# Optimization experiments

Measured on AMD Instinct MI355X. Metric: run time of the kernel, lower is better.

Reference implementation:

```python
import jax, jax.numpy as jnp
import numpy as np

N_NODES = 50000
N_EDGES = 800000
F_IN, F_HID, F_OUT = 128, 64, 32


def setup_inputs() -> dict:
    key = jax.random.key(0)
    k1, k2, k3, k4, k5, k6 = jax.random.split(key, 6)
    x = jax.random.normal(k1, (N_NODES, F_IN), dtype=jnp.float32)
    edge_index = jax.random.randint(k2, (2, N_EDGES), 0, N_NODES, dtype=jnp.int64)
    # Glorot-ish init for the two GCNConv linear layers
    W1 = jax.random.normal(k3, (F_IN, F_HID), dtype=jnp.float32) / np.sqrt(F_IN)
    b1 = jnp.zeros((F_HID,), dtype=jnp.float32)
    W2 = jax.random.normal(k4, (F_HID, F_OUT), dtype=jnp.float32) / np.sqrt(F_HID)
    b2 = jnp.zeros((F_OUT,), dtype=jnp.float32)
    return {"x": x, "edge_index": edge_index, "W1": W1, "b1": b1, "W2": W2, "b2": b2}


def _gcn_conv(x, src, dst, norm, W, b):
    # GCNConv: linear transform, then D^{-1/2}(A+I)D^{-1/2} aggregation
    xw = x @ W                                # [N, F_out]
    msg = xw[src] * norm[:, None]             # [E+N, F_out] gather + scale
    out = jax.ops.segment_sum(msg, dst, num_segments=x.shape[0])
    return out + b


def reference(x, edge_index, W1, b1, W2, b2):
    n = x.shape[0]
    self_loops = jnp.arange(n, dtype=edge_index.dtype)
    src = jnp.concatenate([edge_index[0], self_loops])  # [E+N]
    dst = jnp.concatenate([edge_index[1], self_loops])
    # symmetric degree normalization (self-loops guarantee deg >= 1)
    deg = jax.ops.segment_sum(jnp.ones_like(dst, dtype=x.dtype), dst, num_segments=n)
    dinv = jax.lax.rsqrt(deg)
    norm = dinv[src] * dinv[dst]              # [E+N]

    h = _gcn_conv(x, src, dst, norm, W1, b1)
    h = jax.nn.relu(h)
    # dropout p=0.5 is identity in eval mode (training=False)
    out = _gcn_conv(h, src, dst, norm, W2, b2)
    return out
```

## Files before the change

kernel.cpp:

```cpp
#include <hip/hip_runtime.h>
#include <hip/hip_fp16.h>

#define NN 50000
#define NE 800000
#define F_IN 128
#define F_HID 64
#define F_OUT 32
#define CAP 48
#define NBUCK 196
#define EPB 4096
#define CELL 64
#define NXW1 782

typedef _Float16 f16x8 __attribute__((ext_vector_type(8)));
typedef float f32x4 __attribute__((ext_vector_type(4)));
#define XS_STR 136


__global__ __launch_bounds__(256) void fused_xw1_partition_kernel(
        const float* __restrict__ x, const float* __restrict__ W,
        const int* __restrict__ src, const int* __restrict__ dst,
        int* __restrict__ cnt2t, unsigned int* __restrict__ bstore2,
        __half* __restrict__ outh) {
    __shared__ _Float16 xs[64 * XS_STR];
    __shared__ _Float16 wt[64 * XS_STR];
    __shared__ int hist[4][NBUCK];
    __shared__ int cur[NBUCK];
    int t = threadIdx.x;

    if (blockIdx.x < NBUCK) {
        int blk = blockIdx.x;
        for (int i = t; i < 4 * NBUCK; i += 256) ((int*)hist)[i] = 0;
        __syncthreads();
        int wv = t >> 6;
        int base = blk * EPB;
        unsigned int pk[16];
#pragma unroll
        for (int i = 0; i < 16; ++i) {
            int e = base + i * 256 + t;
            if (e < NE) {
                unsigned int d = (unsigned int)dst[e];
                unsigned int s = (unsigned int)src[e];
                pk[i] = (d << 16) | s;
                atomicAdd(&hist[wv][d >> 8], 1);
            } else {
                pk[i] = 0xFFFFFFFFu;
            }
        }
        __syncthreads();
        for (int b = t; b < NBUCK; b += 256) {
            int h = hist[0][b] + hist[1][b] + hist[2][b] + hist[3][b];
            cur[b] = 0;
            cnt2t[b * NBUCK + blk] = h;
        }
        __syncthreads();
#pragma unroll
        for (int i = 0; i < 16; ++i) {
            unsigned int p = pk[i];
            if (p != 0xFFFFFFFFu) {
                int b = p >> 24;
                int pos = atomicAdd(&cur[b], 1);
                if (pos < CELL) bstore2[((size_t)blk * NBUCK + b) * CELL + pos] = p;
            }
        }
        return;
    }

    int node0 = (blockIdx.x - NBUCK) * 64;

    {
        int r = t >> 2;
        int c0 = (t & 3) * 32;
        int gn = node0 + r;
        if (gn > NN - 1) gn = NN - 1;
        const float4* xrow = (const float4*)(x + (size_t)gn * F_IN);
#pragma unroll
        for (int i = 0; i < 8; ++i) {
            float4 v = xrow[(c0 >> 2) + i];
            _Float16* p = &xs[r * XS_STR + c0 + i * 4];
            p[0] = (_Float16)v.x; p[1] = (_Float16)v.y;
            p[2] = (_Float16)v.z; p[3] = (_Float16)v.w;
        }
    }
#pragma unroll
    for (int i = 0; i < 8; ++i) {
        int idx4 = t + i * 256;
        int k = idx4 >> 4;
        int n0 = (idx4 & 15) << 2;
        float4 v = ((const float4*)W)[idx4];
        wt[(n0 + 0) * XS_STR + k] = (_Float16)v.x;
        wt[(n0 + 1) * XS_STR + k] = (_Float16)v.y;
        wt[(n0 + 2) * XS_STR + k] = (_Float16)v.z;
        wt[(n0 + 3) * XS_STR + k] = (_Float16)v.w;
    }
    __syncthreads();

    int wave = t >> 6;
    int l = t & 63;
    int quad = l >> 4;
    int lm = l & 15;

    f32x4 acc[4] = {{0,0,0,0},{0,0,0,0},{0,0,0,0},{0,0,0,0}};
    const _Float16* abase = &xs[(wave * 16 + lm) * XS_STR + quad * 8];
#pragma unroll
    for (int kk4 = 0; kk4 < 4; ++kk4) {
        int kk = kk4 * 32;
        f16x8 a = *(const f16x8*)(abase + kk);
#pragma unroll
        for (int ft = 0; ft < 4; ++ft) {
            f16x8 b = *(const f16x8*)&wt[(ft * 16 + lm) * XS_STR + kk + quad * 8];
            acc[ft] = __builtin_amdgcn_mfma_f32_16x16x32_f16(a, b, acc[ft], 0, 0, 0);
        }
    }

    __syncthreads();
    _Float16* ot = xs;
#pragma unroll
    for (int ft = 0; ft < 4; ++ft) {
#pragma unroll
        for (int r = 0; r < 4; ++r) {
            int row_l = wave * 16 + quad * 4 + r;
            ot[row_l * 64 + ft * 16 + lm] = (_Float16)acc[ft][r];
        }
    }
    __syncthreads();
#pragma unroll
    for (int i = 0; i < 2; ++i) {
        int idx = t + i * 256;
        int row = idx >> 3;
        int c8 = (idx & 7) * 8;
        int gn = node0 + row;
        if (gn < NN)
            *(uint4*)(outh + (size_t)gn * 64 + c8) = *(const uint4*)&ot[row * 64 + c8];
    }
}


__device__ __forceinline__ void slot_insert(unsigned int p, int* cnt_l,
                                            unsigned short* slot_l) {
    int dl = (p >> 16) & 255;
    int pos = atomicAdd(&cnt_l[dl], 1);
    if (pos < CAP) slot_l[dl * CAP + pos] = (unsigned short)(p & 0xFFFFu);
}

__global__ __launch_bounds__(256) void build_slots_kernel(
        const int* __restrict__ cnt2t, const unsigned int* __restrict__ bstore2,
        unsigned short* __restrict__ slot, int* __restrict__ cnt_g, float* __restrict__ dinv) {
    __shared__ unsigned short slot_l[256 * CAP];
    __shared__ int cnt_l[256];
    int t = threadIdx.x;
    int b = blockIdx.x;
    cnt_l[t] = 0;
    __syncthreads();

    for (int blk = t; blk < NBUCK; blk += 256) {
        int c = cnt2t[b * NBUCK + blk];
        if (c > CELL) c = CELL;
        const unsigned int* seg = bstore2 + ((size_t)blk * NBUCK + b) * CELL;
        int j = 0;
        for (; j + 4 <= c; j += 4) {
            unsigned int p0 = seg[j + 0];
            unsigned int p1 = seg[j + 1];
            unsigned int p2 = seg[j + 2];
            unsigned int p3 = seg[j + 3];
            slot_insert(p0, cnt_l, slot_l);
            slot_insert(p1, cnt_l, slot_l);
            slot_insert(p2, cnt_l, slot_l);
            slot_insert(p3, cnt_l, slot_l);
        }
        for (; j < c; ++j) slot_insert(seg[j], cnt_l, slot_l);
    }
    __syncthreads();

    unsigned int* sg = (unsigned int*)(slot + (size_t)b * 256 * CAP);
    const unsigned int* sl = (const unsigned int*)slot_l;
    for (int j = t; j < 256 * CAP / 2; j += 256) sg[j] = sl[j];

    int n = b * 256 + t;
    if (n < NN) {
        int c = cnt_l[t];
        cnt_g[n] = c;
        dinv[n] = rsqrtf(1.0f + (float)c);
    }
}


__global__ __launch_bounds__(256, 6) void gather64_w2_kernel(
        const __half* __restrict__ xw, const int* __restrict__ cnt,
        const unsigned short* __restrict__ slot, const float* __restrict__ dinv,
        const float* __restrict__ b1, const float* __restrict__ W2,
        __half* __restrict__ hw2h) {
    __shared__ float w2s[F_HID * F_OUT];
    __shared__ float hl[4][F_HID];
    int t = threadIdx.x;
    for (int i = t; i < F_HID * F_OUT / 4; i += 256)
        ((float4*)w2s)[i] = ((const float4*)W2)[i];
    __syncthreads();

    int lane = t & 63;
    int wv = t >> 6;
    int n = blockIdx.x * 4 + wv;
    int st = lane >> 4;
    int fl4 = lane & 15;
    const uint2* base = (const uint2*)xw;
    int deg = cnt[n];
    if (deg > CAP) deg = CAP;
    float din = dinv[n];
    const unsigned short* srow = slot + (size_t)n * CAP;
    uint2 u_self = base[(size_t)n * 16 + fl4];
    float4 bb = ((const float4*)b1)[fl4];
    float a0 = 0, a1 = 0, a2 = 0, a3 = 0;
    int e = st;
    for (; e + 12 < deg; e += 16) {
        int s0 = srow[e];
        int s1 = srow[e + 4];
        int s2 = srow[e + 8];
        int s3 = srow[e + 12];
        float dv0 = dinv[s0], dv1 = dinv[s1], dv2 = dinv[s2], dv3 = dinv[s3];
        uint2 u0 = base[(size_t)s0 * 16 + fl4];
        uint2 u1 = base[(size_t)s1 * 16 + fl4];
        uint2 u2 = base[(size_t)s2 * 16 + fl4];
        uint2 u3 = base[(size_t)s3 * 16 + fl4];
        float2 p0 = __half22float2(*(__half2*)&u0.x), p1 = __half22float2(*(__half2*)&u0.y);
        float2 q0 = __half22float2(*(__half2*)&u1.x), q1 = __half22float2(*(__half2*)&u1.y);
        float2 r0 = __half22float2(*(__half2*)&u2.x), r1 = __half22float2(*(__half2*)&u2.y);
        float2 t0 = __half22float2(*(__half2*)&u3.x), t1 = __half22float2(*(__half2*)&u3.y);
        a0 += dv0 * p0.x + dv1 * q0.x + dv2 * r0.x + dv3 * t0.x;
        a1 += dv0 * p0.y + dv1 * q0.y + dv2 * r0.y + dv3 * t0.y;
        a2 += dv0 * p1.x + dv1 * q1.x + dv2 * r1.x + dv3 * t1.x;
        a3 += dv0 * p1.y + dv1 * q1.y + dv2 * r1.y + dv3 * t1.y;
    }
    for (; e < deg; e += 4) {
        int s = srow[e];
        float dv = dinv[s];
        uint2 u = base[(size_t)s * 16 + fl4];
        float2 p0 = __half22float2(*(__half2*)&u.x);
        float2 p1 = __half22float2(*(__half2*)&u.y);
        a0 += dv * p0.x; a1 += dv * p0.y; a2 += dv * p1.x; a3 += dv * p1.y;
    }
    a0 += __shfl_xor(a0, 16, 64); a1 += __shfl_xor(a1, 16, 64);
    a2 += __shfl_xor(a2, 16, 64); a3 += __shfl_xor(a3, 16, 64);
    a0 += __shfl_xor(a0, 32, 64); a1 += __shfl_xor(a1, 32, 64);
    a2 += __shfl_xor(a2, 32, 64); a3 += __shfl_xor(a3, 32, 64);
    if (st == 0) {
        float2 s0 = __half22float2(*(__half2*)&u_self.x);
        float2 s1 = __half22float2(*(__half2*)&u_self.y);
        float v0 = din * (a0 + din * s0.x) + bb.x;
        float v1 = din * (a1 + din * s0.y) + bb.y;
        float v2 = din * (a2 + din * s1.x) + bb.z;
        float v3 = din * (a3 + din * s1.y) + bb.w;
        float* hr = &hl[wv][fl4 * 4];
        hr[0] = v0 > 0.f ? v0 : 0.f;
        hr[1] = v1 > 0.f ? v1 : 0.f;
        hr[2] = v2 > 0.f ? v2 : 0.f;
        hr[3] = v3 > 0.f ? v3 : 0.f;
    }
    asm volatile("s_waitcnt lgkmcnt(0)" ::: "memory");
    {
        int f = lane & 31;
        int kh = lane >> 5;
        const float* hr = &hl[wv][kh * 32];
        float acc = 0.0f;
#pragma unroll
        for (int k = 0; k < 32; ++k) acc += hr[k] * w2s[(kh * 32 + k) * F_OUT + f];
        acc += __shfl_xor(acc, 32, 64);
        if (kh == 0) hw2h[(size_t)n * F_OUT + f] = __float2half(acc * din);
    }
}


__global__ __launch_bounds__(256, 8) void gather32_kernel(
        const __half* __restrict__ scaled, const int* __restrict__ cnt,
        const unsigned short* __restrict__ slot, const float* __restrict__ dinv,
        const float* __restrict__ bias, float* __restrict__ out) {
    int lane = threadIdx.x & 63;
    int n = blockIdx.x * 4 + (threadIdx.x >> 6);
    if (n >= NN) return;
    int st = lane >> 3;
    int fl4 = lane & 7;
    const uint2* base = (const uint2*)scaled;
    int deg = cnt[n];
    if (deg > CAP) deg = CAP;
    const unsigned short* srow = slot + (size_t)n * CAP;
    uint2 u_self = base[(size_t)n * 8 + fl4];
    float4 b4 = ((const float4*)bias)[fl4];
    float a0 = 0, a1 = 0, a2 = 0, a3 = 0;
    int e = st;
    for (; e + 8 < deg; e += 16) {
        int s0 = srow[e];
        int s1 = srow[e + 8];
        uint2 u0 = base[(size_t)s0 * 8 + fl4];
        uint2 u1 = base[(size_t)s1 * 8 + fl4];
        float2 p0 = __half22float2(*(__half2*)&u0.x);
        float2 p1 = __half22float2(*(__half2*)&u0.y);
        float2 q0 = __half22float2(*(__half2*)&u1.x);
        float2 q1 = __half22float2(*(__half2*)&u1.y);
        a0 += p0.x + q0.x; a1 += p0.y + q0.y;
        a2 += p1.x + q1.x; a3 += p1.y + q1.y;
    }
    for (; e < deg; e += 8) {
        int s = srow[e];
        uint2 u = base[(size_t)s * 8 + fl4];
        float2 p0 = __half22float2(*(__half2*)&u.x);
        float2 p1 = __half22float2(*(__half2*)&u.y);
        a0 += p0.x; a1 += p0.y; a2 += p1.x; a3 += p1.y;
    }
    a0 += __shfl_xor(a0, 8, 64);  a1 += __shfl_xor(a1, 8, 64);
    a2 += __shfl_xor(a2, 8, 64);  a3 += __shfl_xor(a3, 8, 64);
    a0 += __shfl_xor(a0, 16, 64); a1 += __shfl_xor(a1, 16, 64);
    a2 += __shfl_xor(a2, 16, 64); a3 += __shfl_xor(a3, 16, 64);
    a0 += __shfl_xor(a0, 32, 64); a1 += __shfl_xor(a1, 32, 64);
    a2 += __shfl_xor(a2, 32, 64); a3 += __shfl_xor(a3, 32, 64);
    if (st == 0) {
        float2 s0 = __half22float2(*(__half2*)&u_self.x);
        float2 s1 = __half22float2(*(__half2*)&u_self.y);
        float di = dinv[n];
        float4 r;
        r.x = di * (a0 + s0.x) + b4.x;
        r.y = di * (a1 + s0.y) + b4.y;
        r.z = di * (a2 + s1.x) + b4.z;
        r.w = di * (a3 + s1.y) + b4.w;
        ((float4*)out)[(size_t)n * 8 + fl4] = r;
    }
}


extern "C" void kernel_launch(void* const* d_in, const int* in_sizes, int n_in,
                              void* d_out, int out_size, void* d_ws, size_t ws_size,
                              hipStream_t stream) {
    const float* x  = (const float*)d_in[0];
    const int*   ei = (const int*)d_in[1];
    const float* W1 = (const float*)d_in[2];
    const float* b1 = (const float*)d_in[3];
    const float* W2 = (const float*)d_in[4];
    const float* b2 = (const float*)d_in[5];
    const int* src = ei;
    const int* dst = ei + NE;

    float*          ws      = (float*)d_ws;
    float*          dinv    = ws;
    int*            cnt     = (int*)(ws + 50048);
    int*            cnt2t   = (int*)(ws + 100096);
    unsigned int*   bstore2 = (unsigned int*)(ws + 138624);
    unsigned short* slot    = (unsigned short*)(ws + 2597248);
    __half*         xw1h    = (__half*)(ws + 3801472);
    __half*         hw2h    = (__half*)(ws + 5401472);
    float*          out     = (float*)d_out;

    fused_xw1_partition_kernel<<<NBUCK + NXW1, 256, 0, stream>>>(
        x, W1, src, dst, cnt2t, bstore2, xw1h);
    build_slots_kernel<<<NBUCK, 256, 0, stream>>>(cnt2t, bstore2, slot, cnt, dinv);
    gather64_w2_kernel<<<NN / 4, 256, 0, stream>>>(xw1h, cnt, slot, dinv, b1, W2, hw2h);
    gather32_kernel<<<NN / 4, 256, 0, stream>>>(hw2h, cnt, slot, dinv, b2, out);
}
```

Baseline: 149.0 us.

## Prescale xw1 by dinv in build_slots and widen gather loads to 16 bytes

The build_slots kernel now multiplies each row of the fp16 xw1 by its node's dinv after computing degrees. This removes the per-edge dinv[src] lookup and multiply in the first gather. Both gather kernels switch from 8-byte to 16-byte loads per lane with eight accumulators, so more edges are in flight per wave but an extra shuffle-reduction step is needed. gather64's occupancy hint goes from 6 to 8. The prescale adds a read-modify-write pass over xw1 inside the serial build_slots kernel and rounds the scaled values to fp16.

```diff
diff --git a/kernel.cpp b/kernel.cpp
--- a/kernel.cpp
+++ b/kernel.cpp
@@ -145,9 +145,11 @@
 
 __global__ __launch_bounds__(256) void build_slots_kernel(
         const int* __restrict__ cnt2t, const unsigned int* __restrict__ bstore2,
-        unsigned short* __restrict__ slot, int* __restrict__ cnt_g, float* __restrict__ dinv) {
+        unsigned short* __restrict__ slot, int* __restrict__ cnt_g,
+        float* __restrict__ dinv, __half* __restrict__ xw) {
     __shared__ unsigned short slot_l[256 * CAP];
     __shared__ int cnt_l[256];
+    __shared__ float dinv_l[256];
     int t = threadIdx.x;
     int b = blockIdx.x;
     cnt_l[t] = 0;
@@ -177,15 +179,38 @@
     for (int j = t; j < 256 * CAP / 2; j += 256) sg[j] = sl[j];
 
     int n = b * 256 + t;
+    float dv = 0.0f;
     if (n < NN) {
         int c = cnt_l[t];
         cnt_g[n] = c;
-        dinv[n] = rsqrtf(1.0f + (float)c);
-    }
-}
-
-
-__global__ __launch_bounds__(256, 6) void gather64_w2_kernel(
+        dv = rsqrtf(1.0f + (float)c);
+        dinv[n] = dv;
+    }
+    dinv_l[t] = dv;
+    __syncthreads();
+
+    {
+        uint4* xb = (uint4*)(xw + (size_t)b * 256 * 64);
+        int rowlim = NN - b * 256;
+        for (int i = t; i < 2048; i += 256) {
+            int row = i >> 3;
+            if (row < rowlim) {
+                uint4 u = xb[i];
+                float s = dinv_l[row];
+                __half2* h2 = (__half2*)&u;
+#pragma unroll
+                for (int j = 0; j < 4; ++j) {
+                    float2 f = __half22float2(h2[j]);
+                    h2[j] = __float22half2_rn(make_float2(f.x * s, f.y * s));
+                }
+                xb[i] = u;
+            }
+        }
+    }
+}
+
+
+__global__ __launch_bounds__(256, 8) void gather64_w2_kernel(
         const __half* __restrict__ xw, const int* __restrict__ cnt,
         const unsigned short* __restrict__ slot, const float* __restrict__ dinv,
         const float* __restrict__ b1, const float* __restrict__ W2,
@@ -200,60 +225,65 @@
     int lane = t & 63;
     int wv = t >> 6;
     int n = blockIdx.x * 4 + wv;
-    int st = lane >> 4;
-    int fl4 = lane & 15;
-    const uint2* base = (const uint2*)xw;
+    int st = lane >> 3;
+    int fl = lane & 7;
+    const uint4* base = (const uint4*)xw;
     int deg = cnt[n];
     if (deg > CAP) deg = CAP;
     float din = dinv[n];
     const unsigned short* srow = slot + (size_t)n * CAP;
-    uint2 u_self = base[(size_t)n * 16 + fl4];
-    float4 bb = ((const float4*)b1)[fl4];
-    float a0 = 0, a1 = 0, a2 = 0, a3 = 0;
+    uint4 u_self = base[(size_t)n * 8 + fl];
+    float a0 = 0, a1 = 0, a2 = 0, a3 = 0, a4 = 0, a5 = 0, a6 = 0, a7 = 0;
     int e = st;
-    for (; e + 12 < deg; e += 16) {
+    for (; e + 8 < deg; e += 16) {
         int s0 = srow[e];
-        int s1 = srow[e + 4];
-        int s2 = srow[e + 8];
-        int s3 = srow[e + 12];
-        float dv0 = dinv[s0], dv1 = dinv[s1], dv2 = dinv[s2], dv3 = dinv[s3];
-        uint2 u0 = base[(size_t)s0 * 16 + fl4];
-        uint2 u1 = base[(size_t)s1 * 16 + fl4];
-        uint2 u2 = base[(size_t)s2 * 16 + fl4];
-        uint2 u3 = base[(size_t)s3 * 16 + fl4];
-        float2 p0 = __half22float2(*(__half2*)&u0.x), p1 = __half22float2(*(__half2*)&u0.y);
-        float2 q0 = __half22float2(*(__half2*)&u1.x), q1 = __half22float2(*(__half2*)&u1.y);
-        float2 r0 = __half22float2(*(__half2*)&u2.x), r1 = __half22float2(*(__half2*)&u2.y);
-        float2 t0 = __half22float2(*(__half2*)&u3.x), t1 = __half22float2(*(__half2*)&u3.y);
-        a0 += dv0 * p0.x + dv1 * q0.x + dv2 * r0.x + dv3 * t0.x;
-        a1 += dv0 * p0.y + dv1 * q0.y + dv2 * r0.y + dv3 * t0.y;
-        a2 += dv0 * p1.x + dv1 * q1.x + dv2 * r1.x + dv3 * t1.x;
-        a3 += dv0 * p1.y + dv1 * q1.y + dv2 * r1.y + dv3 * t1.y;
-    }
-    for (; e < deg; e += 4) {
+        int s1 = srow[e + 8];
+        uint4 u0 = base[(size_t)s0 * 8 + fl];
+        uint4 u1 = base[(size_t)s1 * 8 + fl];
+        float2 p;
+        p = __half22float2(*(__half2*)&u0.x); a0 += p.x; a1 += p.y;
+        p = __half22float2(*(__half2*)&u0.y); a2 += p.x; a3 += p.y;
+        p = __half22float2(*(__half2*)&u0.z); a4 += p.x; a5 += p.y;
+        p = __half22float2(*(__half2*)&u0.w); a6 += p.x; a7 += p.y;
+        p = __half22float2(*(__half2*)&u1.x); a0 += p.x; a1 += p.y;
+        p = __half22float2(*(__half2*)&u1.y); a2 += p.x; a3 += p.y;
+        p = __half22float2(*(__half2*)&u1.z); a4 += p.x; a5 += p.y;
+        p = __half22float2(*(__half2*)&u1.w); a6 += p.x; a7 += p.y;
+    }
+    for (; e < deg; e += 8) {
         int s = srow[e];
-        float dv = dinv[s];
-        uint2 u = base[(size_t)s * 16 + fl4];
-        float2 p0 = __half22float2(*(__half2*)&u.x);
-        float2 p1 = __half22float2(*(__half2*)&u.y);
-        a0 += dv * p0.x; a1 += dv * p0.y; a2 += dv * p1.x; a3 += dv * p1.y;
-    }
-    a0 += __shfl_xor(a0, 16, 64); a1 += __shfl_xor(a1, 16, 64);
-    a2 += __shfl_xor(a2, 16, 64); a3 += __shfl_xor(a3, 16, 64);
-    a0 += __shfl_xor(a0, 32, 64); a1 += __shfl_xor(a1, 32, 64);
-    a2 += __shfl_xor(a2, 32, 64); a3 += __shfl_xor(a3, 32, 64);
+        uint4 u = base[(size_t)s * 8 + fl];
+        float2 p;
+        p = __half22float2(*(__half2*)&u.x); a0 += p.x; a1 += p.y;
+        p = __half22float2(*(__half2*)&u.y); a2 += p.x; a3 += p.y;
+        p = __half22float2(*(__half2*)&u.z); a4 += p.x; a5 += p.y;
+        p = __half22float2(*(__half2*)&u.w); a6 += p.x; a7 += p.y;
+    }
+#define RED64(S) \
+    a0 += __shfl_xor(a0, S, 64); a1 += __shfl_xor(a1, S, 64); \
+    a2 += __shfl_xor(a2, S, 64); a3 += __shfl_xor(a3, S, 64); \
+    a4 += __shfl_xor(a4, S, 64); a5 += __shfl_xor(a5, S, 64); \
+    a6 += __shfl_xor(a6, S, 64); a7 += __shfl_xor(a7, S, 64);
+    RED64(8) RED64(16) RED64(32)
+#undef RED64
     if (st == 0) {
-        float2 s0 = __half22float2(*(__half2*)&u_self.x);
-        float2 s1 = __half22float2(*(__half2*)&u_self.y);
-        float v0 = din * (a0 + din * s0.x) + bb.x;
-        float v1 = din * (a1 + din * s0.y) + bb.y;
-        float v2 = din * (a2 + din * s1.x) + bb.z;
-        float v3 = din * (a3 + din * s1.y) + bb.w;
-        float* hr = &hl[wv][fl4 * 4];
-        hr[0] = v0 > 0.f ? v0 : 0.f;
-        hr[1] = v1 > 0.f ? v1 : 0.f;
-        hr[2] = v2 > 0.f ? v2 : 0.f;
-        hr[3] = v3 > 0.f ? v3 : 0.f;
+        float2 p;
+        p = __half22float2(*(__half2*)&u_self.x); a0 += p.x; a1 += p.y;
+        p = __half22float2(*(__half2*)&u_self.y); a2 += p.x; a3 += p.y;
+        p = __half22float2(*(__half2*)&u_self.z); a4 += p.x; a5 += p.y;
+        p = __half22float2(*(__half2*)&u_self.w); a6 += p.x; a7 += p.y;
+        float4 bb0 = ((const float4*)b1)[fl * 2];
+        float4 bb1 = ((const float4*)b1)[fl * 2 + 1];
+        float* hr = &hl[wv][fl * 8];
+        float v;
+        v = din * a0 + bb0.x; hr[0] = v > 0.f ? v : 0.f;
+        v = din * a1 + bb0.y; hr[1] = v > 0.f ? v : 0.f;
+        v = din * a2 + bb0.z; hr[2] = v > 0.f ? v : 0.f;
+        v = din * a3 + bb0.w; hr[3] = v > 0.f ? v : 0.f;
+        v = din * a4 + bb1.x; hr[4] = v > 0.f ? v : 0.f;
+        v = din * a5 + bb1.y; hr[5] = v > 0.f ? v : 0.f;
+        v = din * a6 + bb1.z; hr[6] = v > 0.f ? v : 0.f;
+        v = din * a7 + bb1.w; hr[7] = v > 0.f ? v : 0.f;
     }
     asm volatile("s_waitcnt lgkmcnt(0)" ::: "memory");
     {
@@ -276,51 +306,66 @@
     int lane = threadIdx.x & 63;
     int n = blockIdx.x * 4 + (threadIdx.x >> 6);
     if (n >= NN) return;
-    int st = lane >> 3;
-    int fl4 = lane & 7;
-    const uint2* base = (const uint2*)scaled;
+    int st = lane >> 2;
+    int fl = lane & 3;
+    const uint4* base = (const uint4*)scaled;
     int deg = cnt[n];
     if (deg > CAP) deg = CAP;
     const unsigned short* srow = slot + (size_t)n * CAP;
-    uint2 u_self = base[(size_t)n * 8 + fl4];
-    float4 b4 = ((const float4*)bias)[fl4];
-    float a0 = 0, a1 = 0, a2 = 0, a3 = 0;
+    uint4 u_self = base[(size_t)n * 4 + fl];
+    float a0 = 0, a1 = 0, a2 = 0, a3 = 0, a4 = 0, a5 = 0, a6 = 0, a7 = 0;
     int e = st;
-    for (; e + 8 < deg; e += 16) {
+    for (; e + 16 < deg; e += 32) {
         int s0 = srow[e];
-        int s1 = srow[e + 8];
-        uint2 u0 = base[(size_t)s0 * 8 + fl4];
-        uint2 u1 = base[(size_t)s1 * 8 + fl4];
-        float2 p0 = __half22float2(*(__half2*)&u0.x);
-        float2 p1 = __half22float2(*(__half2*)&u0.y);
-        float2 q0 = __half22float2(*(__half2*)&u1.x);
-        float2 q1 = __half22float2(*(__half2*)&u1.y);
-        a0 += p0.x + q0.x; a1 += p0.y + q0.y;
-        a2 += p1.x + q1.x; a3 += p1.y + q1.y;
-    }
-    for (; e < deg; e += 8) {
+        int s1 = srow[e + 16];
+        uint4 u0 = base[(size_t)s0 * 4 + fl];
+        uint4 u1 = base[(size_t)s1 * 4 + fl];
+        float2 p;
+        p = __half22float2(*(__half2*)&u0.x); a0 += p.x; a1 += p.y;
+        p = __half22float2(*(__half2*)&u0.y); a2 += p.x; a3 += p.y;
+        p = __half22float2(*(__half2*)&u0.z); a4 += p.x; a5 += p.y;
+        p = __half22float2(*(__half2*)&u0.w); a6 += p.x; a7 += p.y;
+        p = __half22float2(*(__half2*)&u1.x); a0 += p.x; a1 += p.y;
+        p = __half22float2(*(__half2*)&u1.y); a2 += p.x; a3 += p.y;
+        p = __half22float2(*(__half2*)&u1.z); a4 += p.x; a5 += p.y;
+        p = __half22float2(*(__half2*)&u1.w); a6 += p.x; a7 += p.y;
+    }
+    for (; e < deg; e += 16) {
         int s = srow[e];
-        uint2 u = base[(size_t)s * 8 + fl4];
-        float2 p0 = __half22float2(*(__half2*)&u.x);
-        float2 p1 = __half22float2(*(__half2*)&u.y);
-        a0 += p0.x; a1 += p0.y; a2 += p1.x; a3 += p1.y;
-    }
-    a0 += __shfl_xor(a0, 8, 64);  a1 += __shfl_xor(a1, 8, 64);
-    a2 += __shfl_xor(a2, 8, 64);  a3 += __shfl_xor(a3, 8, 64);
-    a0 += __shfl_xor(a0, 16, 64); a1 += __shfl_xor(a1, 16, 64);
-    a2 += __shfl_xor(a2, 16, 64); a3 += __shfl_xor(a3, 16, 64);
-    a0 += __shfl_xor(a0, 32, 64); a1 += __shfl_xor(a1, 32, 64);
-    a2 += __shfl_xor(a2, 32, 64); a3 += __shfl_xor(a3, 32, 64);
+        uint4 u = base[(size_t)s * 4 + fl];
+        float2 p;
+        p = __half22float2(*(__half2*)&u.x); a0 += p.x; a1 += p.y;
+        p = __half22float2(*(__half2*)&u.y); a2 += p.x; a3 += p.y;
+        p = __half22float2(*(__half2*)&u.z); a4 += p.x; a5 += p.y;
+        p = __half22float2(*(__half2*)&u.w); a6 += p.x; a7 += p.y;
+    }
+#define RED32(S) \
+    a0 += __shfl_xor(a0, S, 64); a1 += __shfl_xor(a1, S, 64); \
+    a2 += __shfl_xor(a2, S, 64); a3 += __shfl_xor(a3, S, 64); \
+    a4 += __shfl_xor(a4, S, 64); a5 += __shfl_xor(a5, S, 64); \
+    a6 += __shfl_xor(a6, S, 64); a7 += __shfl_xor(a7, S, 64);
+    RED32(4) RED32(8) RED32(16) RED32(32)
+#undef RED32
     if (st == 0) {
-        float2 s0 = __half22float2(*(__half2*)&u_self.x);
-        float2 s1 = __half22float2(*(__half2*)&u_self.y);
+        float2 p;
+        p = __half22float2(*(__half2*)&u_self.x); a0 += p.x; a1 += p.y;
+        p = __half22float2(*(__half2*)&u_self.y); a2 += p.x; a3 += p.y;
+        p = __half22float2(*(__half2*)&u_self.z); a4 += p.x; a5 += p.y;
+        p = __half22float2(*(__half2*)&u_self.w); a6 += p.x; a7 += p.y;
         float di = dinv[n];
-        float4 r;
-        r.x = di * (a0 + s0.x) + b4.x;
-        r.y = di * (a1 + s0.y) + b4.y;
-        r.z = di * (a2 + s1.x) + b4.z;
-        r.w = di * (a3 + s1.y) + b4.w;
-        ((float4*)out)[(size_t)n * 8 + fl4] = r;
+        float4 b40 = ((const float4*)bias)[fl * 2];
+        float4 b41 = ((const float4*)bias)[fl * 2 + 1];
+        float4 r0, r1;
+        r0.x = di * a0 + b40.x;
+        r0.y = di * a1 + b40.y;
+        r0.z = di * a2 + b40.z;
+        r0.w = di * a3 + b40.w;
+        r1.x = di * a4 + b41.x;
+        r1.y = di * a5 + b41.y;
+        r1.z = di * a6 + b41.z;
+        r1.w = di * a7 + b41.w;
+        ((float4*)out)[(size_t)n * 8 + fl * 2] = r0;
+        ((float4*)out)[(size_t)n * 8 + fl * 2 + 1] = r1;
     }
 }
 
@@ -349,7 +394,7 @@
 
     fused_xw1_partition_kernel<<<NBUCK + NXW1, 256, 0, stream>>>(
         x, W1, src, dst, cnt2t, bstore2, xw1h);
-    build_slots_kernel<<<NBUCK, 256, 0, stream>>>(cnt2t, bstore2, slot, cnt, dinv);
+    build_slots_kernel<<<NBUCK, 256, 0, stream>>>(cnt2t, bstore2, slot, cnt, dinv, xw1h);
     gather64_w2_kernel<<<NN / 4, 256, 0, stream>>>(xw1h, cnt, slot, dinv, b1, W2, hw2h);
     gather32_kernel<<<NN / 4, 256, 0, stream>>>(hw2h, cnt, slot, dinv, b2, out);
 }
```

Result: slower. 158.9 us (+6.6%).

## Replace two-pass bucketed edge partition with direct global-atomic slot scatter

Applied to the files above, without the earlier changes.

Removes the bucket histogram/partition pass and the separate build_slots kernel. Edges are now scattered straight into per-node slot lists with global atomicAdd on per-node counters, zeroed by a memset. The dinv array is dropped, and rsqrt(1+deg) is recomputed from the counts inside the gather kernels. This saves a kernel launch and an intermediate buffer, at the cost of contended global atomics and scattered 2-byte stores. Slot order within each node also becomes nondeterministic.

```diff
diff --git a/kernel.cpp b/kernel.cpp
--- a/kernel.cpp
+++ b/kernel.cpp
@@ -7,9 +7,7 @@
 #define F_HID 64
 #define F_OUT 32
 #define CAP 48
-#define NBUCK 196
-#define EPB 4096
-#define CELL 64
+#define NSCAT 782
 #define NXW1 782
 
 typedef _Float16 f16x8 __attribute__((ext_vector_type(8)));
@@ -17,56 +15,44 @@
 #define XS_STR 136
 
 
-__global__ __launch_bounds__(256) void fused_xw1_partition_kernel(
+__global__ __launch_bounds__(256) void fused_xw1_scatter_kernel(
         const float* __restrict__ x, const float* __restrict__ W,
         const int* __restrict__ src, const int* __restrict__ dst,
-        int* __restrict__ cnt2t, unsigned int* __restrict__ bstore2,
+        int* __restrict__ cnt, unsigned short* __restrict__ slot,
         __half* __restrict__ outh) {
     __shared__ _Float16 xs[64 * XS_STR];
     __shared__ _Float16 wt[64 * XS_STR];
-    __shared__ int hist[4][NBUCK];
-    __shared__ int cur[NBUCK];
     int t = threadIdx.x;
 
-    if (blockIdx.x < NBUCK) {
-        int blk = blockIdx.x;
-        for (int i = t; i < 4 * NBUCK; i += 256) ((int*)hist)[i] = 0;
-        __syncthreads();
-        int wv = t >> 6;
-        int base = blk * EPB;
-        unsigned int pk[16];
-#pragma unroll
-        for (int i = 0; i < 16; ++i) {
-            int e = base + i * 256 + t;
-            if (e < NE) {
-                unsigned int d = (unsigned int)dst[e];
-                unsigned int s = (unsigned int)src[e];
-                pk[i] = (d << 16) | s;
-                atomicAdd(&hist[wv][d >> 8], 1);
-            } else {
-                pk[i] = 0xFFFFFFFFu;
+    if (blockIdx.x < NSCAT) {
+        int e0 = blockIdx.x * 1024 + t * 4;
+        if (e0 + 3 < NE) {
+            int4 d4 = *(const int4*)(dst + e0);
+            int4 s4 = *(const int4*)(src + e0);
+            int p0 = atomicAdd(&cnt[d4.x], 1);
+            if (p0 < CAP) slot[(size_t)d4.x * CAP + p0] = (unsigned short)s4.x;
+            int p1 = atomicAdd(&cnt[d4.y], 1);
+            if (p1 < CAP) slot[(size_t)d4.y * CAP + p1] = (unsigned short)s4.y;
+            int p2 = atomicAdd(&cnt[d4.z], 1);
+            if (p2 < CAP) slot[(size_t)d4.z * CAP + p2] = (unsigned short)s4.z;
+            int p3 = atomicAdd(&cnt[d4.w], 1);
+            if (p3 < CAP) slot[(size_t)d4.w * CAP + p3] = (unsigned short)s4.w;
+        } else {
+#pragma unroll
+            for (int i = 0; i < 4; ++i) {
+                int e = e0 + i;
+                if (e < NE) {
+                    int d = dst[e];
+                    int s = src[e];
+                    int pos = atomicAdd(&cnt[d], 1);
+                    if (pos < CAP) slot[(size_t)d * CAP + pos] = (unsigned short)s;
+                }
             }
         }
-        __syncthreads();
-        for (int b = t; b < NBUCK; b += 256) {
-            int h = hist[0][b] + hist[1][b] + hist[2][b] + hist[3][b];
-            cur[b] = 0;
-            cnt2t[b * NBUCK + blk] = h;
-        }
-        __syncthreads();
-#pragma unroll
-        for (int i = 0; i < 16; ++i) {
-            unsigned int p = pk[i];
-            if (p != 0xFFFFFFFFu) {
-                int b = p >> 24;
-                int pos = atomicAdd(&cur[b], 1);
-                if (pos < CELL) bstore2[((size_t)blk * NBUCK + b) * CELL + pos] = p;
-            }
-        }
         return;
     }
 
-    int node0 = (blockIdx.x - NBUCK) * 64;
+    int node0 = (blockIdx.x - NSCAT) * 64;
 
     {
         int r = t >> 2;
@@ -136,58 +122,9 @@
 }
 
 
-__device__ __forceinline__ void slot_insert(unsigned int p, int* cnt_l,
-                                            unsigned short* slot_l) {
-    int dl = (p >> 16) & 255;
-    int pos = atomicAdd(&cnt_l[dl], 1);
-    if (pos < CAP) slot_l[dl * CAP + pos] = (unsigned short)(p & 0xFFFFu);
-}
-
-__global__ __launch_bounds__(256) void build_slots_kernel(
-        const int* __restrict__ cnt2t, const unsigned int* __restrict__ bstore2,
-        unsigned short* __restrict__ slot, int* __restrict__ cnt_g, float* __restrict__ dinv) {
-    __shared__ unsigned short slot_l[256 * CAP];
-    __shared__ int cnt_l[256];
-    int t = threadIdx.x;
-    int b = blockIdx.x;
-    cnt_l[t] = 0;
-    __syncthreads();
-
-    for (int blk = t; blk < NBUCK; blk += 256) {
-        int c = cnt2t[b * NBUCK + blk];
-        if (c > CELL) c = CELL;
-        const unsigned int* seg = bstore2 + ((size_t)blk * NBUCK + b) * CELL;
-        int j = 0;
-        for (; j + 4 <= c; j += 4) {
-            unsigned int p0 = seg[j + 0];
-            unsigned int p1 = seg[j + 1];
-            unsigned int p2 = seg[j + 2];
-            unsigned int p3 = seg[j + 3];
-            slot_insert(p0, cnt_l, slot_l);
-            slot_insert(p1, cnt_l, slot_l);
-            slot_insert(p2, cnt_l, slot_l);
-            slot_insert(p3, cnt_l, slot_l);
-        }
-        for (; j < c; ++j) slot_insert(seg[j], cnt_l, slot_l);
-    }
-    __syncthreads();
-
-    unsigned int* sg = (unsigned int*)(slot + (size_t)b * 256 * CAP);
-    const unsigned int* sl = (const unsigned int*)slot_l;
-    for (int j = t; j < 256 * CAP / 2; j += 256) sg[j] = sl[j];
-
-    int n = b * 256 + t;
-    if (n < NN) {
-        int c = cnt_l[t];
-        cnt_g[n] = c;
-        dinv[n] = rsqrtf(1.0f + (float)c);
-    }
-}
-
-
 __global__ __launch_bounds__(256, 6) void gather64_w2_kernel(
         const __half* __restrict__ xw, const int* __restrict__ cnt,
-        const unsigned short* __restrict__ slot, const float* __restrict__ dinv,
+        const unsigned short* __restrict__ slot,
         const float* __restrict__ b1, const float* __restrict__ W2,
         __half* __restrict__ hw2h) {
     __shared__ float w2s[F_HID * F_OUT];
@@ -203,9 +140,9 @@
     int st = lane >> 4;
     int fl4 = lane & 15;
     const uint2* base = (const uint2*)xw;
-    int deg = cnt[n];
-    if (deg > CAP) deg = CAP;
-    float din = dinv[n];
+    int deg_raw = cnt[n];
+    int deg = deg_raw > CAP ? CAP : deg_raw;
+    float din = rsqrtf(1.0f + (float)deg_raw);
     const unsigned short* srow = slot + (size_t)n * CAP;
     uint2 u_self = base[(size_t)n * 16 + fl4];
     float4 bb = ((const float4*)b1)[fl4];
@@ -216,11 +153,15 @@
         int s1 = srow[e + 4];
         int s2 = srow[e + 8];
         int s3 = srow[e + 12];
-        float dv0 = dinv[s0], dv1 = dinv[s1], dv2 = dinv[s2], dv3 = dinv[s3];
+        int c0 = cnt[s0], c1 = cnt[s1], c2 = cnt[s2], c3 = cnt[s3];
         uint2 u0 = base[(size_t)s0 * 16 + fl4];
         uint2 u1 = base[(size_t)s1 * 16 + fl4];
         uint2 u2 = base[(size_t)s2 * 16 + fl4];
         uint2 u3 = base[(size_t)s3 * 16 + fl4];
+        float dv0 = rsqrtf(1.0f + (float)c0);
+        float dv1 = rsqrtf(1.0f + (float)c1);
+        float dv2 = rsqrtf(1.0f + (float)c2);
+        float dv3 = rsqrtf(1.0f + (float)c3);
         float2 p0 = __half22float2(*(__half2*)&u0.x), p1 = __half22float2(*(__half2*)&u0.y);
         float2 q0 = __half22float2(*(__half2*)&u1.x), q1 = __half22float2(*(__half2*)&u1.y);
         float2 r0 = __half22float2(*(__half2*)&u2.x), r1 = __half22float2(*(__half2*)&u2.y);
@@ -232,8 +173,9 @@
     }
     for (; e < deg; e += 4) {
         int s = srow[e];
-        float dv = dinv[s];
+        int c = cnt[s];
         uint2 u = base[(size_t)s * 16 + fl4];
+        float dv = rsqrtf(1.0f + (float)c);
         float2 p0 = __half22float2(*(__half2*)&u.x);
         float2 p1 = __half22float2(*(__half2*)&u.y);
         a0 += dv * p0.x; a1 += dv * p0.y; a2 += dv * p1.x; a3 += dv * p1.y;
@@ -271,7 +213,7 @@
 
 __global__ __launch_bounds__(256, 8) void gather32_kernel(
         const __half* __restrict__ scaled, const int* __restrict__ cnt,
-        const unsigned short* __restrict__ slot, const float* __restrict__ dinv,
+        const unsigned short* __restrict__ slot,
         const float* __restrict__ bias, float* __restrict__ out) {
     int lane = threadIdx.x & 63;
     int n = blockIdx.x * 4 + (threadIdx.x >> 6);
@@ -279,8 +221,8 @@
     int st = lane >> 3;
     int fl4 = lane & 7;
     const uint2* base = (const uint2*)scaled;
-    int deg = cnt[n];
-    if (deg > CAP) deg = CAP;
+    int deg_raw = cnt[n];
+    int deg = deg_raw > CAP ? CAP : deg_raw;
     const unsigned short* srow = slot + (size_t)n * CAP;
     uint2 u_self = base[(size_t)n * 8 + fl4];
     float4 b4 = ((const float4*)bias)[fl4];
@@ -314,7 +256,7 @@
     if (st == 0) {
         float2 s0 = __half22float2(*(__half2*)&u_self.x);
         float2 s1 = __half22float2(*(__half2*)&u_self.y);
-        float di = dinv[n];
+        float di = rsqrtf(1.0f + (float)deg_raw);
         float4 r;
         r.x = di * (a0 + s0.x) + b4.x;
         r.y = di * (a1 + s0.y) + b4.y;
@@ -337,19 +279,16 @@
     const int* src = ei;
     const int* dst = ei + NE;
 
-    float*          ws      = (float*)d_ws;
-    float*          dinv    = ws;
-    int*            cnt     = (int*)(ws + 50048);
-    int*            cnt2t   = (int*)(ws + 100096);
-    unsigned int*   bstore2 = (unsigned int*)(ws + 138624);
-    unsigned short* slot    = (unsigned short*)(ws + 2597248);
-    __half*         xw1h    = (__half*)(ws + 3801472);
-    __half*         hw2h    = (__half*)(ws + 5401472);
-    float*          out     = (float*)d_out;
-
-    fused_xw1_partition_kernel<<<NBUCK + NXW1, 256, 0, stream>>>(
-        x, W1, src, dst, cnt2t, bstore2, xw1h);
-    build_slots_kernel<<<NBUCK, 256, 0, stream>>>(cnt2t, bstore2, slot, cnt, dinv);
-    gather64_w2_kernel<<<NN / 4, 256, 0, stream>>>(xw1h, cnt, slot, dinv, b1, W2, hw2h);
-    gather32_kernel<<<NN / 4, 256, 0, stream>>>(hw2h, cnt, slot, dinv, b2, out);
-}
+    float*          ws    = (float*)d_ws;
+    int*            cnt   = (int*)ws;
+    unsigned short* slot  = (unsigned short*)(ws + 50048);
+    __half*         xw1h  = (__half*)(ws + 1250048);
+    __half*         hw2h  = (__half*)(ws + 2850048);
+    float*          out   = (float*)d_out;
+
+    hipMemsetAsync(cnt, 0, NN * sizeof(int), stream);
+    fused_xw1_scatter_kernel<<<NSCAT + NXW1, 256, 0, stream>>>(
+        x, W1, src, dst, cnt, slot, xw1h);
+    gather64_w2_kernel<<<NN / 4, 256, 0, stream>>>(xw1h, cnt, slot, b1, W2, hw2h);
+    gather32_kernel<<<NN / 4, 256, 0, stream>>>(hw2h, cnt, slot, b2, out);
+}
```

After: 200.7 us. +34.7%, slower.
